# Optimization experiments

Measured on AMD Instinct MI355X. Metric: run time of the kernel, lower is better.

The kernel has to match this reference:

```python
import jax, jax.numpy as jnp
import numpy as np

D_MODEL = 1024
N_HEAD = 16
SEQ_LEN = 4096


def setup_inputs() -> dict:
    key = jax.random.key(0)
    ks = jax.random.split(key, 5)
    s = 0.02
    return {
        "x": jax.random.normal(ks[0], (SEQ_LEN, D_MODEL), dtype=jnp.float32),
        "w_qkv": jax.random.normal(ks[1], (D_MODEL, 3 * D_MODEL), dtype=jnp.float32) * s,
        "b_qkv": jnp.zeros((3 * D_MODEL,), dtype=jnp.float32),
        "w_o": jax.random.normal(ks[2], (D_MODEL, D_MODEL), dtype=jnp.float32) * s,
        "b_o": jnp.zeros((D_MODEL,), dtype=jnp.float32),
    }


def reference(x, w_qkv, b_qkv, w_o, b_o):
    seq_len, d_model = x.shape
    n_head = N_HEAD
    d_h = d_model // n_head

    qkv = x @ w_qkv + b_qkv                                  # [S, 3D]
    q, k, v = jnp.split(qkv, 3, axis=-1)                     # each [S, D]
    # [S, D] -> [H, S, d_h]
    q = q.reshape(seq_len, n_head, d_h).transpose(1, 0, 2)
    k = k.reshape(seq_len, n_head, d_h).transpose(1, 0, 2)
    v = v.reshape(seq_len, n_head, d_h).transpose(1, 0, 2)

    sim = jnp.einsum("hsd,htd->hst", q, k) / jnp.sqrt(jnp.float32(d_h))  # [H, S, S]
    causal = jnp.tril(jnp.ones((seq_len, seq_len), dtype=bool))[None]    # [1, S, S]
    neg_inf = jnp.finfo(sim.dtype).min
    sim = jnp.where(causal, sim, neg_inf)
    attn = jax.nn.softmax(sim, axis=-1)                                  # [H, S, S]
    out = jnp.einsum("hst,htd->hsd", attn, v)                            # [H, S, d_h]
    out = out.transpose(1, 0, 2).reshape(seq_len, d_model)               # [S, D]
    return out @ w_o + b_o
```

## Files before the change

kernel.cpp:

```cpp
#include <hip/hip_runtime.h>
#include <hip/hip_bf16.h>
#include <stdint.h>

typedef __bf16 bf16_t;
typedef __bf16 bf16x8 __attribute__((ext_vector_type(8)));
typedef float f32x4 __attribute__((ext_vector_type(4)));
typedef float f32x16 __attribute__((ext_vector_type(16)));
typedef unsigned uint2e __attribute__((ext_vector_type(2)));

#define SEQ_LEN 4096
#define D_MODEL 1024
#define N_HEAD 16



__device__ __forceinline__ void gload_lds16(const void* g, void* lds) {
  __builtin_amdgcn_global_load_lds(
      (__attribute__((address_space(1))) void*)(g),
      (__attribute__((address_space(3))) void*)(lds), 16, 0, 0);
}

__device__ __forceinline__ unsigned short f2bfu(float f) {
  __bf16 h = (__bf16)f;
  return __builtin_bit_cast(unsigned short, h);
}

__device__ __forceinline__ unsigned cvt_pk_bf16(float a, float b) {
  unsigned r;
  asm("v_cvt_pk_bf16_f32 %0, %1, %2" : "=v"(r) : "v"(a), "v"(b));
  return r;
}

#define CBAR() asm volatile("" ::: "memory")


__global__ __launch_bounds__(256) void prep_fused(const float* __restrict__ x,
                                                  bf16_t* __restrict__ xh,
                                                  const float* __restrict__ w_qkv,
                                                  bf16_t* __restrict__ wqkvT,
                                                  const float* __restrict__ w_o,
                                                  bf16_t* __restrict__ woT) {
  __shared__ float tile[64][65];
  const int b = blockIdx.x;
  if (b < 4096) {
    int i = (b * 256 + threadIdx.x) * 4;
    float4 v = *(const float4*)(x + i);
    unsigned int lo = (unsigned)f2bfu(v.x) | ((unsigned)f2bfu(v.y) << 16);
    unsigned int hi = (unsigned)f2bfu(v.z) | ((unsigned)f2bfu(v.w) << 16);
    uint2 pk; pk.x = lo; pk.y = hi;
    *(uint2*)(xh + i) = pk;
    return;
  }
  const float* W;
  bf16_t* Wt;
  int C, bi;
  if (b < 4864) { W = w_qkv; Wt = wqkvT; C = 3072; bi = b - 4096; }
  else          { W = w_o;   Wt = woT;   C = 1024; bi = b - 4864; }
  const int R = 1024;
  const int tc = C >> 6;
  const int bc = bi % tc;
  const int br = bi / tc;
  #pragma unroll
  for (int p = 0; p < 16; ++p) {
    int idx = p * 256 + threadIdx.x;
    int i = idx >> 6, j = idx & 63;
    tile[i][j] = W[(size_t)(br * 64 + i) * C + bc * 64 + j];
  }
  __syncthreads();
  #pragma unroll
  for (int p = 0; p < 16; ++p) {
    int idx = p * 256 + threadIdx.x;
    int jj = idx >> 6, ii = idx & 63;
    Wt[(size_t)(bc * 64 + jj) * R + br * 64 + ii] = (bf16_t)tile[ii][jj];
  }
}


__device__ __forceinline__ void stage_half(const bf16_t* src, char* ldsbase,
                                           int w, int srow, int schunk) {
  const bf16_t* s0 = src + (size_t)(w * 8 + srow) * 1024 + schunk * 8;
  char* d0 = ldsbase + w * 1024;
  gload_lds16(s0, d0);
  gload_lds16(s0 + 64 * 1024, d0 + 8192);
}

__global__ __launch_bounds__(512, 2) void gemm1_8p(const bf16_t* __restrict__ A,
                                                   const bf16_t* __restrict__ Bt,
                                                   const float* __restrict__ bias,
                                                   bf16_t* __restrict__ qfout,
                                                   bf16_t* __restrict__ kfout,
                                                   bf16_t* __restrict__ vfout) {
  __shared__ char ldsbuf[131072];
  const int tid = threadIdx.x;
  const int lane = tid & 63;
  const int w = tid >> 6;
  const int wm = w >> 2;
  const int wn = w & 3;
  const int i16 = lane & 15;
  const int g = lane >> 4;
  const int hi = lane >> 5;
  const int bswz = (blockIdx.x & 7) * 24 + (blockIdx.x >> 3);
  const int bm = bswz / 12;
  const int bn = bswz % 12;

  const int srow = lane >> 3;
  const int schunk = (lane & 7) ^ (hi << 1);
  const int s5 = ((i16 >> 2) & 1) << 5;

  auto stA = [&](int buf, int half, int kt) {
    stage_half(A + (size_t)(bm * 256 + half * 128) * 1024 + kt * 64,
               ldsbuf + buf * 32768 + half * 16384, w, srow, schunk);
  };
  auto stB = [&](int buf, int half, int kt) {
    stage_half(Bt + (size_t)(bn * 256 + half * 128) * 1024 + kt * 64,
               ldsbuf + 65536 + buf * 32768 + half * 16384, w, srow, schunk);
  };

  f32x4 acc[8][4];
  #pragma unroll
  for (int m = 0; m < 8; ++m)
    #pragma unroll
    for (int n = 0; n < 4; ++n)
      acc[m][n] = (f32x4){0.f, 0.f, 0.f, 0.f};

  const int browbase = (wn & 1) * 64;

  stA(0, 0, 0); stA(0, 1, 0); stB(0, 0, 0); stB(0, 1, 0);
  stB(1, 0, 1); stB(1, 1, 1);
  asm volatile("s_waitcnt vmcnt(4)" ::: "memory");
  CBAR(); __builtin_amdgcn_s_barrier(); CBAR();

  bf16x8 bfr[4][2];

  for (int i = 0; i < 8; ++i) {
    const int t1 = 2 * i + 1, t2 = 2 * i + 2, t3 = 2 * i + 3;
    #pragma unroll
    for (int p = 0; p < 8; ++p) {
      const int buf = p >> 2;
      const int q = p & 3;
      const char* aB = ldsbuf + buf * 32768 + wm * 16384;
      const char* bB = ldsbuf + 65536 + buf * 32768 + (wn >> 1) * 16384;
      if (q == 0) {
        #pragma unroll
        for (int n = 0; n < 4; ++n)
          #pragma unroll
          for (int ks = 0; ks < 2; ++ks) {
            int U = (browbase + n * 16 + i16) * 128 + ks * 64 + g * 16;
            bfr[n][ks] = *(const bf16x8*)(bB + (U ^ s5));
          }
      }
      bf16x8 af[2][2];
      #pragma unroll
      for (int mm = 0; mm < 2; ++mm)
        #pragma unroll
        for (int ks = 0; ks < 2; ++ks) {
          int U = ((q * 2 + mm) * 16 + i16) * 128 + ks * 64 + g * 16;
          af[mm][ks] = *(const bf16x8*)(aB + (U ^ s5));
        }
      if (p == 0)      stA(1, 0, t1);
      else if (p == 1) stA(1, 1, t1);
      else if (p == 2) { if (t2 < 16) stB(0, 0, t2); }
      else if (p == 3) { if (t2 < 16) stB(0, 1, t2); }
      else if (p == 4) { if (t2 < 16) stA(0, 0, t2); }
      else if (p == 5) { if (t2 < 16) stA(0, 1, t2); }
      else if (p == 6) { if (t3 < 16) stB(1, 0, t3); }
      else             { if (t3 < 16) stB(1, 1, t3); }

      CBAR(); __builtin_amdgcn_s_barrier(); CBAR();

      __builtin_amdgcn_s_setprio(1);
      #pragma unroll
      for (int mm = 0; mm < 2; ++mm)
        #pragma unroll
        for (int n = 0; n < 4; ++n)
          #pragma unroll
          for (int ks = 0; ks < 2; ++ks)
            acc[q * 2 + mm][n] = __builtin_amdgcn_mfma_f32_16x16x32_bf16(
                af[mm][ks], bfr[n][ks], acc[q * 2 + mm][n], 0, 0, 0);
      __builtin_amdgcn_s_setprio(0);

      if (p == 3) {
        if (i == 7) asm volatile("s_waitcnt vmcnt(0)" ::: "memory");
        else        asm volatile("s_waitcnt vmcnt(4)" ::: "memory");
      } else if (p == 7 && i < 7) {
        asm volatile("s_waitcnt vmcnt(4)" ::: "memory");
      }
      CBAR(); __builtin_amdgcn_s_barrier(); CBAR();
    }
  }

  #pragma unroll
  for (int m = 0; m < 8; ++m) {
    #pragma unroll
    for (int n = 0; n < 4; ++n) {
      int col = bn * 256 + wn * 64 + n * 16 + i16;
      float bv = bias[col];
      int row0 = bm * 256 + wm * 128 + m * 16 + g * 4;
      if (col < 2048) {
        const bool isK = (col >= 1024);
        const float scl = isK ? 0.18033688011112042f : 1.0f;
        bf16_t* base = isK ? kfout : qfout;
        int dg = col & 1023;
        int hh = dg >> 6, d = dg & 63;
        int ks = d >> 4, hib = (d >> 3) & 1, e = d & 7;
        int t = row0 >> 5, l0 = row0 & 31;
        bf16_t* fp = base + (size_t)hh * 262144 + t * 2048 + ks * 512 +
                     hib * 256 + l0 * 8 + e;
        #pragma unroll
        for (int r = 0; r < 4; ++r)
          fp[r * 8] = (bf16_t)((acc[m][n][r] + bv) * scl);
      } else {
        int dg = col - 2048;
        int hh = dg >> 6, dh = dg & 63;
        int dt = dh >> 5, l31v = dh & 31;
        int t = row0 >> 5, inner = row0 & 31;
        int g2 = inner >> 4, hiv = (inner >> 3) & 1, e0 = inner & 7;
        uint2 pk;
        pk.x = cvt_pk_bf16(acc[m][n][0] + bv, acc[m][n][1] + bv);
        pk.y = cvt_pk_bf16(acc[m][n][2] + bv, acc[m][n][3] + bv);
        *(uint2*)(vfout + (size_t)hh * 262144 + t * 2048 + dt * 1024 +
                  g2 * 512 + hiv * 256 + l31v * 8 + e0) = pk;
      }
    }
  }
}


__global__ __launch_bounds__(256) void gemm_bt(const bf16_t* __restrict__ A,
                                               const bf16_t* __restrict__ Bt,
                                               const float* __restrict__ bias,
                                               float* __restrict__ Cout,
                                               int M, int N, int K) {
  __shared__ bf16_t As[128 * 32];
  __shared__ bf16_t Bs[128 * 32];
  const int tid = threadIdx.x;
  const int lane = tid & 63;
  const int w = tid >> 6;
  const int wr = (w >> 1) * 64;
  const int wc = (w & 1) * 64;
  const int i16 = lane & 15;
  const int g = lane >> 4;
  const int ntn = N >> 7;
  const int nwg = gridDim.x;
  const int bswz = (blockIdx.x & 7) * (nwg >> 3) + (blockIdx.x >> 3);
  const int bm = bswz / ntn;
  const int bn = bswz % ntn;
  const bf16_t* Abase = A + (size_t)(bm * 128) * K;
  const bf16_t* Bbase = Bt + (size_t)(bn * 128) * K;

  f32x4 acc[4][4];
  #pragma unroll
  for (int m = 0; m < 4; ++m)
    #pragma unroll
    for (int n = 0; n < 4; ++n)
      acc[m][n] = (f32x4){0.f, 0.f, 0.f, 0.f};

  for (int kt = 0; kt < K; kt += 32) {
    __syncthreads();
    #pragma unroll
    for (int p = 0; p < 2; ++p) {
      int idx = p * 256 + tid;
      int row = idx >> 2, ch = idx & 3;
      gload_lds16(Abase + (size_t)row * K + kt + ch * 8, (char*)As + idx * 16);
      gload_lds16(Bbase + (size_t)row * K + kt + ch * 8, (char*)Bs + idx * 16);
    }
    __syncthreads();
    bf16x8 af[4], bq[4];
    #pragma unroll
    for (int m = 0; m < 4; ++m)
      af[m] = *(const bf16x8*)(As + (wr + m * 16 + i16) * 32 + g * 8);
    #pragma unroll
    for (int n = 0; n < 4; ++n)
      bq[n] = *(const bf16x8*)(Bs + (wc + n * 16 + i16) * 32 + g * 8);
    #pragma unroll
    for (int m = 0; m < 4; ++m)
      #pragma unroll
      for (int n = 0; n < 4; ++n)
        acc[m][n] = __builtin_amdgcn_mfma_f32_16x16x32_bf16(af[m], bq[n], acc[m][n], 0, 0, 0);
  }

  #pragma unroll
  for (int m = 0; m < 4; ++m) {
    #pragma unroll
    for (int n = 0; n < 4; ++n) {
      int col = bn * 128 + wc + n * 16 + i16;
      float bv = bias ? bias[col] : 0.f;
      int row0 = bm * 128 + wr + m * 16 + g * 4;
      #pragma unroll
      for (int r = 0; r < 4; ++r)
        Cout[(size_t)(row0 + r) * N + col] = acc[m][n][r] + bv;
    }
  }
}


__global__ __launch_bounds__(256) void attn_fwd(const bf16_t* __restrict__ qf_,
                                                const bf16_t* __restrict__ kf,
                                                const bf16_t* __restrict__ vf,
                                                bf16_t* __restrict__ aout) {
  __shared__ float Obuf[2][32][68];
  __shared__ float lpart[4][2][32];
  const int tid = threadIdx.x;
  const int w = tid >> 6;
  const int lane = tid & 63;
  const int l31 = lane & 31;
  const int hi = lane >> 5;
  const int bid = blockIdx.x;
  const int h = ((bid & 7) << 1) | ((bid >> 3) & 1);
  const int j = 127 - (bid >> 4);
  const int qg0 = j * 32;

  const bf16_t* qp = qf_ + (size_t)h * 262144 + (size_t)j * 2048 + hi * 256 + l31 * 8;
  bf16x8 qf[4];
  #pragma unroll
  for (int ks = 0; ks < 4; ++ks)
    qf[ks] = *(const bf16x8*)(qp + ks * 512);

  const bf16_t* kp = kf + (size_t)h * 262144 + hi * 256 + l31 * 8;
  const bf16_t* vp = vf + (size_t)h * 262144 + hi * 256 + l31 * 8;

  f32x16 ot0, ot1;
  #pragma unroll
  for (int r = 0; r < 16; ++r) { ot0[r] = 0.f; ot1[r] = 0.f; }
  float l_run = 0.f;

  const int nt = j + 1;
  bf16x8 kc[4], kn[4], vc[4];
  #pragma unroll
  for (int ks = 0; ks < 4; ++ks) {
    kc[ks] = *(const bf16x8*)(kp + w * 2048 + ks * 512);
    kn[ks] = kc[ks];
  }

  for (int t = w; t < nt; t += 4) {
    #pragma unroll
    for (int i = 0; i < 4; ++i) {
      int dt = i >> 1, g2 = i & 1;
      vc[i] = *(const bf16x8*)(vp + (size_t)t * 2048 + dt * 1024 + g2 * 512);
    }
    if (t + 4 < nt) {
      #pragma unroll
      for (int ks = 0; ks < 4; ++ks)
        kn[ks] = *(const bf16x8*)(kp + (size_t)(t + 4) * 2048 + ks * 512);
    }

    f32x16 s;
    #pragma unroll
    for (int r = 0; r < 16; ++r) s[r] = 0.f;
    __builtin_amdgcn_s_setprio(1);
    #pragma unroll
    for (int ks = 0; ks < 4; ++ks)
      s = __builtin_amdgcn_mfma_f32_32x32x16_bf16(kc[ks], qf[ks], s, 0, 0, 0);
    __builtin_amdgcn_s_setprio(0);

    if (t == nt - 1) {
      #pragma unroll
      for (int r = 0; r < 16; ++r) {
        int c = (r & 3) + 8 * (r >> 2) + 4 * hi;
        if (c > l31) s[r] = -1e30f;
      }
    }

    #pragma unroll
    for (int r = 0; r < 16; ++r)
      s[r] = __builtin_amdgcn_exp2f(s[r]);

    float sm[8];
    #pragma unroll
    for (int r = 0; r < 8; ++r) sm[r] = s[r] + s[r + 8];
    #pragma unroll
    for (int r = 0; r < 4; ++r) sm[r] = sm[r] + sm[r + 4];
    l_run += (sm[0] + sm[1]) + (sm[2] + sm[3]);

    bf16x8 pb[2];
    #pragma unroll
    for (int g2 = 0; g2 < 2; ++g2) {
      const int r0 = g2 * 8;
      unsigned a0 = cvt_pk_bf16(s[r0 + 0], s[r0 + 1]);
      unsigned a1 = cvt_pk_bf16(s[r0 + 2], s[r0 + 3]);
      unsigned b0 = cvt_pk_bf16(s[r0 + 4], s[r0 + 5]);
      unsigned b1 = cvt_pk_bf16(s[r0 + 6], s[r0 + 7]);
      uint2e p0 = __builtin_amdgcn_permlane32_swap(a0, b0, false, false);
      uint2e p1 = __builtin_amdgcn_permlane32_swap(a1, b1, false, false);
      uint4 f;
      f.x = p0[0];
      f.y = p1[0];
      f.z = p0[1];
      f.w = p1[1];
      pb[g2] = __builtin_bit_cast(bf16x8, f);
    }

    __builtin_amdgcn_s_setprio(1);
    ot0 = __builtin_amdgcn_mfma_f32_32x32x16_bf16(vc[0], pb[0], ot0, 0, 0, 0);
    ot0 = __builtin_amdgcn_mfma_f32_32x32x16_bf16(vc[1], pb[1], ot0, 0, 0, 0);
    ot1 = __builtin_amdgcn_mfma_f32_32x32x16_bf16(vc[2], pb[0], ot1, 0, 0, 0);
    ot1 = __builtin_amdgcn_mfma_f32_32x32x16_bf16(vc[3], pb[1], ot1, 0, 0, 0);
    __builtin_amdgcn_s_setprio(0);

    #pragma unroll
    for (int ks = 0; ks < 4; ++ks) kc[ks] = kn[ks];
  }

  lpart[w][hi][l31] = l_run;
  if (w >= 2) {
    #pragma unroll
    for (int dt = 0; dt < 2; ++dt) {
      const f32x16& o = dt ? ot1 : ot0;
      #pragma unroll
      for (int rq = 0; rq < 4; ++rq) {
        f32x4 qd;
        qd[0] = o[4 * rq + 0];
        qd[1] = o[4 * rq + 1];
        qd[2] = o[4 * rq + 2];
        qd[3] = o[4 * rq + 3];
        *(f32x4*)&Obuf[w - 2][l31][dt * 32 + 8 * rq + 4 * hi] = qd;
      }
    }
  }
  __syncthreads();
  if (w < 2) {
    #pragma unroll
    for (int dt = 0; dt < 2; ++dt) {
      const f32x16& o = dt ? ot1 : ot0;
      #pragma unroll
      for (int rq = 0; rq < 4; ++rq) {
        f32x4 qd = *(const f32x4*)&Obuf[w][l31][dt * 32 + 8 * rq + 4 * hi];
        qd[0] += o[4 * rq + 0];
        qd[1] += o[4 * rq + 1];
        qd[2] += o[4 * rq + 2];
        qd[3] += o[4 * rq + 3];
        *(f32x4*)&Obuf[w][l31][dt * 32 + 8 * rq + 4 * hi] = qd;
      }
    }
  }
  __syncthreads();
  #pragma unroll
  for (int iter = 0; iter < 8; ++iter) {
    int qq = w * 8 + iter;
    float sum = Obuf[0][qq][lane] + Obuf[1][qq][lane];
    float lst = lpart[0][0][qq] + lpart[0][1][qq] + lpart[1][0][qq] + lpart[1][1][qq] +
                lpart[2][0][qq] + lpart[2][1][qq] + lpart[3][0][qq] + lpart[3][1][qq];
    aout[(size_t)(qg0 + qq) * 1024 + h * 64 + lane] = (bf16_t)(sum / lst);
  }
}


extern "C" void kernel_launch(void* const* d_in, const int* in_sizes, int n_in,
                              void* d_out, int out_size, void* d_ws, size_t ws_size,
                              hipStream_t stream) {
  const float* x     = (const float*)d_in[0];
  const float* w_qkv = (const float*)d_in[1];
  const float* b_qkv = (const float*)d_in[2];
  const float* w_o   = (const float*)d_in[3];
  const float* b_o   = (const float*)d_in[4];

  char* ws = (char*)d_ws;
  bf16_t* xh    = (bf16_t*)(ws);
  bf16_t* wqkvT = (bf16_t*)(ws + 8388608);
  bf16_t* woT   = (bf16_t*)(ws + 14680064);
  bf16_t* qfb   = (bf16_t*)(ws + 16777216);
  bf16_t* kfb   = (bf16_t*)(ws + 25165824);
  bf16_t* vfb   = (bf16_t*)(ws + 33554432);
  bf16_t* aout  = (bf16_t*)(ws + 41943040);

  prep_fused<<<5120, 256, 0, stream>>>(x, xh, w_qkv, wqkvT, w_o, woT);

  gemm1_8p<<<192, 512, 0, stream>>>(xh, wqkvT, b_qkv, qfb, kfb, vfb);

  attn_fwd<<<N_HEAD * (SEQ_LEN / 32), 256, 0, stream>>>(qfb, kfb, vfb, aout);

  gemm_bt<<<(4096 / 128) * (1024 / 128), 256, 0, stream>>>(
      aout, woT, b_o, (float*)d_out, 4096, 1024, 1024);
}
```

Measured before the change: 130.5 us.

## Share K/V tiles via double-buffered LDS across four query-tile waves

The attention kernel changes from one 32-query block split across four waves over keys to a 128-query block where each wave owns its own 32 queries. K/V tiles are loaded once per block into double-buffered LDS with global_load_lds and shared by all waves, which cuts global K/V traffic about fourfold. The cross-wave output reduction through LDS is gone, and each wave normalises and writes its own output directly. In exchange, a __syncthreads sits in every key step, the causal imbalance across waves leaves early waves idle, and the grid shrinks to 512 blocks.

```diff
diff --git a/kernel.cpp b/kernel.cpp
--- a/kernel.cpp
+++ b/kernel.cpp
@@ -298,8 +298,8 @@
                                                 const bf16_t* __restrict__ kf,
                                                 const bf16_t* __restrict__ vf,
                                                 bf16_t* __restrict__ aout) {
-  __shared__ float Obuf[2][32][68];
-  __shared__ float lpart[4][2][32];
+  __shared__ __align__(16) bf16_t Ks[2][2048];
+  __shared__ __align__(16) bf16_t Vs[2][2048];
   const int tid = threadIdx.x;
   const int w = tid >> 6;
   const int lane = tid & 63;
@@ -307,140 +307,123 @@
   const int hi = lane >> 5;
   const int bid = blockIdx.x;
   const int h = ((bid & 7) << 1) | ((bid >> 3) & 1);
-  const int j = 127 - (bid >> 4);
-  const int qg0 = j * 32;
-
-  const bf16_t* qp = qf_ + (size_t)h * 262144 + (size_t)j * 2048 + hi * 256 + l31 * 8;
+  const int J = 31 - (bid >> 4);
+  const int jw = 4 * J + w;
+  const int q = J * 128 + w * 32 + l31;
+
+  const bf16_t* qp = qf_ + (size_t)h * 262144 + (size_t)jw * 2048 + hi * 256 + l31 * 8;
   bf16x8 qf[4];
   #pragma unroll
   for (int ks = 0; ks < 4; ++ks)
     qf[ks] = *(const bf16x8*)(qp + ks * 512);
 
-  const bf16_t* kp = kf + (size_t)h * 262144 + hi * 256 + l31 * 8;
-  const bf16_t* vp = vf + (size_t)h * 262144 + hi * 256 + l31 * 8;
+  const bf16_t* kh = kf + (size_t)h * 262144;
+  const bf16_t* vh = vf + (size_t)h * 262144;
 
   f32x16 ot0, ot1;
   #pragma unroll
   for (int r = 0; r < 16; ++r) { ot0[r] = 0.f; ot1[r] = 0.f; }
   float l_run = 0.f;
 
-  const int nt = j + 1;
-  bf16x8 kc[4], kn[4], vc[4];
-  #pragma unroll
-  for (int ks = 0; ks < 4; ++ks) {
-    kc[ks] = *(const bf16x8*)(kp + w * 2048 + ks * 512);
-    kn[ks] = kc[ks];
-  }
-
-  for (int t = w; t < nt; t += 4) {
-    #pragma unroll
-    for (int i = 0; i < 4; ++i) {
-      int dt = i >> 1, g2 = i & 1;
-      vc[i] = *(const bf16x8*)(vp + (size_t)t * 2048 + dt * 1024 + g2 * 512);
-    }
-    if (t + 4 < nt) {
+  const int ntb = 4 * J + 4;
+  const int lfb = lane >> 5;
+  (void)lfb;
+
+  gload_lds16(kh + tid * 8, (char*)Ks[0] + tid * 16);
+  gload_lds16(vh + tid * 8, (char*)Vs[0] + tid * 16);
+  __syncthreads();
+  int cur = 0;
+
+  for (int t = 0; t < ntb; ++t) {
+    if (t + 1 < ntb) {
+      gload_lds16(kh + (size_t)(t + 1) * 2048 + tid * 8, (char*)Ks[cur ^ 1] + tid * 16);
+      gload_lds16(vh + (size_t)(t + 1) * 2048 + tid * 8, (char*)Vs[cur ^ 1] + tid * 16);
+    }
+
+    if (t <= jw) {
+      const char* Kc = (const char*)Ks[cur];
+      const char* Vc = (const char*)Vs[cur];
+
+      bf16x8 kfr[4];
       #pragma unroll
       for (int ks = 0; ks < 4; ++ks)
-        kn[ks] = *(const bf16x8*)(kp + (size_t)(t + 4) * 2048 + ks * 512);
-    }
-
-    f32x16 s;
-    #pragma unroll
-    for (int r = 0; r < 16; ++r) s[r] = 0.f;
-    __builtin_amdgcn_s_setprio(1);
-    #pragma unroll
-    for (int ks = 0; ks < 4; ++ks)
-      s = __builtin_amdgcn_mfma_f32_32x32x16_bf16(kc[ks], qf[ks], s, 0, 0, 0);
-    __builtin_amdgcn_s_setprio(0);
-
-    if (t == nt - 1) {
-      #pragma unroll
-      for (int r = 0; r < 16; ++r) {
-        int c = (r & 3) + 8 * (r >> 2) + 4 * hi;
-        if (c > l31) s[r] = -1e30f;
-      }
-    }
-
-    #pragma unroll
-    for (int r = 0; r < 16; ++r)
-      s[r] = __builtin_amdgcn_exp2f(s[r]);
-
-    float sm[8];
-    #pragma unroll
-    for (int r = 0; r < 8; ++r) sm[r] = s[r] + s[r + 8];
-    #pragma unroll
-    for (int r = 0; r < 4; ++r) sm[r] = sm[r] + sm[r + 4];
-    l_run += (sm[0] + sm[1]) + (sm[2] + sm[3]);
-
-    bf16x8 pb[2];
-    #pragma unroll
-    for (int g2 = 0; g2 < 2; ++g2) {
-      const int r0 = g2 * 8;
-      unsigned a0 = cvt_pk_bf16(s[r0 + 0], s[r0 + 1]);
-      unsigned a1 = cvt_pk_bf16(s[r0 + 2], s[r0 + 3]);
-      unsigned b0 = cvt_pk_bf16(s[r0 + 4], s[r0 + 5]);
-      unsigned b1 = cvt_pk_bf16(s[r0 + 6], s[r0 + 7]);
-      uint2e p0 = __builtin_amdgcn_permlane32_swap(a0, b0, false, false);
-      uint2e p1 = __builtin_amdgcn_permlane32_swap(a1, b1, false, false);
-      uint4 f;
-      f.x = p0[0];
-      f.y = p1[0];
-      f.z = p0[1];
-      f.w = p1[1];
-      pb[g2] = __builtin_bit_cast(bf16x8, f);
-    }
-
-    __builtin_amdgcn_s_setprio(1);
-    ot0 = __builtin_amdgcn_mfma_f32_32x32x16_bf16(vc[0], pb[0], ot0, 0, 0, 0);
-    ot0 = __builtin_amdgcn_mfma_f32_32x32x16_bf16(vc[1], pb[1], ot0, 0, 0, 0);
-    ot1 = __builtin_amdgcn_mfma_f32_32x32x16_bf16(vc[2], pb[0], ot1, 0, 0, 0);
-    ot1 = __builtin_amdgcn_mfma_f32_32x32x16_bf16(vc[3], pb[1], ot1, 0, 0, 0);
-    __builtin_amdgcn_s_setprio(0);
-
-    #pragma unroll
-    for (int ks = 0; ks < 4; ++ks) kc[ks] = kn[ks];
-  }
-
-  lpart[w][hi][l31] = l_run;
-  if (w >= 2) {
-    #pragma unroll
-    for (int dt = 0; dt < 2; ++dt) {
-      const f32x16& o = dt ? ot1 : ot0;
-      #pragma unroll
-      for (int rq = 0; rq < 4; ++rq) {
-        f32x4 qd;
-        qd[0] = o[4 * rq + 0];
-        qd[1] = o[4 * rq + 1];
-        qd[2] = o[4 * rq + 2];
-        qd[3] = o[4 * rq + 3];
-        *(f32x4*)&Obuf[w - 2][l31][dt * 32 + 8 * rq + 4 * hi] = qd;
-      }
-    }
-  }
-  __syncthreads();
-  if (w < 2) {
-    #pragma unroll
-    for (int dt = 0; dt < 2; ++dt) {
-      const f32x16& o = dt ? ot1 : ot0;
-      #pragma unroll
-      for (int rq = 0; rq < 4; ++rq) {
-        f32x4 qd = *(const f32x4*)&Obuf[w][l31][dt * 32 + 8 * rq + 4 * hi];
-        qd[0] += o[4 * rq + 0];
-        qd[1] += o[4 * rq + 1];
-        qd[2] += o[4 * rq + 2];
-        qd[3] += o[4 * rq + 3];
-        *(f32x4*)&Obuf[w][l31][dt * 32 + 8 * rq + 4 * hi] = qd;
-      }
-    }
-  }
-  __syncthreads();
-  #pragma unroll
-  for (int iter = 0; iter < 8; ++iter) {
-    int qq = w * 8 + iter;
-    float sum = Obuf[0][qq][lane] + Obuf[1][qq][lane];
-    float lst = lpart[0][0][qq] + lpart[0][1][qq] + lpart[1][0][qq] + lpart[1][1][qq] +
-                lpart[2][0][qq] + lpart[2][1][qq] + lpart[3][0][qq] + lpart[3][1][qq];
-    aout[(size_t)(qg0 + qq) * 1024 + h * 64 + lane] = (bf16_t)(sum / lst);
+        kfr[ks] = *(const bf16x8*)(Kc + ks * 1024 + hi * 512 + l31 * 16);
+
+      f32x16 s;
+      #pragma unroll
+      for (int r = 0; r < 16; ++r) s[r] = 0.f;
+      __builtin_amdgcn_s_setprio(1);
+      #pragma unroll
+      for (int ks = 0; ks < 4; ++ks)
+        s = __builtin_amdgcn_mfma_f32_32x32x16_bf16(kfr[ks], qf[ks], s, 0, 0, 0);
+      __builtin_amdgcn_s_setprio(0);
+
+      if (t == jw) {
+        #pragma unroll
+        for (int r = 0; r < 16; ++r) {
+          int c = (r & 3) + 8 * (r >> 2) + 4 * hi;
+          if (c > l31) s[r] = -1e30f;
+        }
+      }
+
+      #pragma unroll
+      for (int r = 0; r < 16; ++r)
+        s[r] = __builtin_amdgcn_exp2f(s[r]);
+
+      float sm[8];
+      #pragma unroll
+      for (int r = 0; r < 8; ++r) sm[r] = s[r] + s[r + 8];
+      #pragma unroll
+      for (int r = 0; r < 4; ++r) sm[r] = sm[r] + sm[r + 4];
+      l_run += (sm[0] + sm[1]) + (sm[2] + sm[3]);
+
+      bf16x8 pb[2];
+      #pragma unroll
+      for (int g2 = 0; g2 < 2; ++g2) {
+        const int r0 = g2 * 8;
+        unsigned a0 = cvt_pk_bf16(s[r0 + 0], s[r0 + 1]);
+        unsigned a1 = cvt_pk_bf16(s[r0 + 2], s[r0 + 3]);
+        unsigned b0 = cvt_pk_bf16(s[r0 + 4], s[r0 + 5]);
+        unsigned b1 = cvt_pk_bf16(s[r0 + 6], s[r0 + 7]);
+        uint2e p0 = __builtin_amdgcn_permlane32_swap(a0, b0, false, false);
+        uint2e p1 = __builtin_amdgcn_permlane32_swap(a1, b1, false, false);
+        uint4 f;
+        f.x = p0[0];
+        f.y = p1[0];
+        f.z = p0[1];
+        f.w = p1[1];
+        pb[g2] = __builtin_bit_cast(bf16x8, f);
+      }
+
+      __builtin_amdgcn_s_setprio(1);
+      {
+        bf16x8 v0 = *(const bf16x8*)(Vc + 0 * 2048 + 0 * 1024 + hi * 512 + l31 * 16);
+        bf16x8 v1 = *(const bf16x8*)(Vc + 0 * 2048 + 1 * 1024 + hi * 512 + l31 * 16);
+        bf16x8 v2 = *(const bf16x8*)(Vc + 1 * 2048 + 0 * 1024 + hi * 512 + l31 * 16);
+        bf16x8 v3 = *(const bf16x8*)(Vc + 1 * 2048 + 1 * 1024 + hi * 512 + l31 * 16);
+        ot0 = __builtin_amdgcn_mfma_f32_32x32x16_bf16(v0, pb[0], ot0, 0, 0, 0);
+        ot0 = __builtin_amdgcn_mfma_f32_32x32x16_bf16(v1, pb[1], ot0, 0, 0, 0);
+        ot1 = __builtin_amdgcn_mfma_f32_32x32x16_bf16(v2, pb[0], ot1, 0, 0, 0);
+        ot1 = __builtin_amdgcn_mfma_f32_32x32x16_bf16(v3, pb[1], ot1, 0, 0, 0);
+      }
+      __builtin_amdgcn_s_setprio(0);
+    }
+
+    __syncthreads();
+    cur ^= 1;
+  }
+
+  float inv = 1.0f / (l_run + __shfl_xor(l_run, 32));
+  #pragma unroll
+  for (int dt = 0; dt < 2; ++dt) {
+    const f32x16& o = dt ? ot1 : ot0;
+    #pragma unroll
+    for (int rq = 0; rq < 4; ++rq) {
+      unsigned lo = cvt_pk_bf16(o[4 * rq + 0] * inv, o[4 * rq + 1] * inv);
+      unsigned hi2 = cvt_pk_bf16(o[4 * rq + 2] * inv, o[4 * rq + 3] * inv);
+      uint2 pk2; pk2.x = lo; pk2.y = hi2;
+      *(uint2*)(aout + (size_t)q * 1024 + h * 64 + dt * 32 + 8 * rq + 4 * hi) = pk2;
+    }
   }
 }
 
@@ -467,7 +450,7 @@
 
   gemm1_8p<<<192, 512, 0, stream>>>(xh, wqkvT, b_qkv, qfb, kfb, vfb);
 
-  attn_fwd<<<N_HEAD * (SEQ_LEN / 32), 256, 0, stream>>>(qfb, kfb, vfb, aout);
+  attn_fwd<<<N_HEAD * (SEQ_LEN / 128), 256, 0, stream>>>(qfb, kfb, vfb, aout);
 
   gemm_bt<<<(4096 / 128) * (1024 / 128), 256, 0, stream>>>(
       aout, woT, b_o, (float*)d_out, 4096, 1024, 1024);
```

Result: slower. 187.2 us (+43.5%).
